# Kernel optimization log

Measured on AMD Instinct MI355X. Metric: run time of the kernel, lower is better.

The kernel has to match this reference:

```python
import jax, jax.numpy as jnp
import numpy as np

N = 10000        # nodes
E = 320000       # edges (before self-loops)
IN = 128         # in_channels
HID = 128        # hidden_channels per head
HEADS = 4
OUT = 512        # out_channels (final layer, 1 head, no concat)
SLOPE = 0.2      # PyG GATConv negative_slope default


def setup_inputs() -> dict:
    key = jax.random.key(0)
    ks = jax.random.split(key, 16)
    s = 0.05
    inp = {
        "x": jax.random.normal(ks[0], (N, IN), dtype=jnp.float32),
        "edge_index": jax.random.randint(ks[1], (2, E), 0, N, dtype=jnp.int32),
        # layer 1: IN -> HEADS*HID, concat
        "W1": jax.random.normal(ks[2], (IN, HEADS * HID), dtype=jnp.float32) * s,
        "a_src1": jax.random.normal(ks[3], (1, HEADS, HID), dtype=jnp.float32) * s,
        "a_dst1": jax.random.normal(ks[4], (1, HEADS, HID), dtype=jnp.float32) * s,
        "b1": jnp.zeros((HEADS * HID,), dtype=jnp.float32),
        # layer 2: HEADS*HID -> HEADS*HID, concat
        "W2": jax.random.normal(ks[5], (HEADS * HID, HEADS * HID), dtype=jnp.float32) * s,
        "a_src2": jax.random.normal(ks[6], (1, HEADS, HID), dtype=jnp.float32) * s,
        "a_dst2": jax.random.normal(ks[7], (1, HEADS, HID), dtype=jnp.float32) * s,
        "b2": jnp.zeros((HEADS * HID,), dtype=jnp.float32),
        # layer 3: HEADS*HID -> OUT, heads=1, mean (no concat)
        "W3": jax.random.normal(ks[8], (HEADS * HID, OUT), dtype=jnp.float32) * s,
        "a_src3": jax.random.normal(ks[9], (1, 1, OUT), dtype=jnp.float32) * s,
        "a_dst3": jax.random.normal(ks[10], (1, 1, OUT), dtype=jnp.float32) * s,
        "b3": jnp.zeros((OUT,), dtype=jnp.float32),
    }
    return inp


def gat_layer(x, src, dst, W, a_src, a_dst, bias, heads, ch, concat):
    n = x.shape[0]
    h = (x @ W).reshape(n, heads, ch)                 # [N,H,C]
    al_s = jnp.sum(h * a_src, axis=-1)                # [N,H]
    al_d = jnp.sum(h * a_dst, axis=-1)                # [N,H]
    logits = jax.nn.leaky_relu(al_s[src] + al_d[dst], SLOPE)  # [E,H]
    # segment softmax over incoming edges of each destination node
    logits = logits - jax.ops.segment_max(logits, dst, num_segments=n)[dst]
    e = jnp.exp(logits)
    denom = jax.ops.segment_sum(e, dst, num_segments=n)[dst]
    alpha = e / denom                                  # [E,H]
    out = jax.ops.segment_sum(h[src] * alpha[:, :, None], dst, num_segments=n)  # [N,H,C]
    out = out.reshape(n, heads * ch) if concat else out.mean(axis=1)
    return out + bias


def reference(x, edge_index, W1, a_src1, a_dst1, b1, W2, a_src2, a_dst2, b2,
              W3, a_src3, a_dst3, b3):
    n = x.shape[0]
    loop = jnp.arange(n, dtype=edge_index.dtype)       # PyG add_self_loops=True
    src = jnp.concatenate([edge_index[0], loop])
    dst = jnp.concatenate([edge_index[1], loop])
    h = jax.nn.relu(gat_layer(x, src, dst, W1, a_src1, a_dst1, b1, HEADS, HID, True))
    h = jax.nn.relu(gat_layer(h, src, dst, W2, a_src2, a_dst2, b2, HEADS, HID, True))
    return gat_layer(h, src, dst, W3, a_src3, a_dst3, b3, 1, OUT, False)
```

## Files before the change

### kernel.cpp

```cpp
#include <hip/hip_runtime.h>

#define NSLOPE 0.2f
#define CAP 128

typedef __bf16 bf16x8 __attribute__((ext_vector_type(8)));
typedef __bf16 bf16x4 __attribute__((ext_vector_type(4)));
typedef __bf16 bf16x2 __attribute__((ext_vector_type(2)));
typedef float  f32x4  __attribute__((ext_vector_type(4)));

typedef uint32_t __attribute__((address_space(1))) gbl_u32;
typedef uint32_t __attribute__((address_space(3))) lds_u32;

__global__ void fill_kernel(const int* __restrict__ ei, int E,
                            int* cnt, int* __restrict__ col){
  int i = blockIdx.x*blockDim.x + threadIdx.x;
  if (i < E){
    int s = ei[i], d = ei[E + i];
    int slot = atomicAdd(&cnt[d], 1);
    if (slot < CAP) col[(d << 7) + slot] = s;
  }
}

__device__ __forceinline__ void wsplit_body(
    const float* __restrict__ W, __bf16* __restrict__ Bt, int K, int Nc,
    int kb, int nb, float (*hi_s)[33], float (*lo_s)[33]){
  int tx = threadIdx.x & 31, ty = threadIdx.x >> 5;
  int k0 = kb * 32, n0 = nb * 32;
#pragma unroll
  for (int i = 0; i < 4; i++){
    int r = ty + i*8;
    float v = W[(size_t)(k0 + r)*Nc + n0 + tx];
    float h = (float)(__bf16)v;
    hi_s[r][tx] = h;
    lo_s[r][tx] = v - h;
  }
  __syncthreads();
  int K2 = 2*K;
#pragma unroll
  for (int i = 0; i < 4; i++){
    int n = ty + i*8;
    Bt[(size_t)(n0 + n)*K2 + k0 + tx]     = (__bf16)hi_s[tx][n];
    Bt[(size_t)(n0 + n)*K2 + K + k0 + tx] = (__bf16)lo_s[tx][n];
  }
}

__global__ __launch_bounds__(256) void prep_kernel(
    const float* __restrict__ x, __bf16* __restrict__ X2,
    const float* __restrict__ W1, __bf16* __restrict__ B1t,
    const float* __restrict__ W2, __bf16* __restrict__ B2t,
    const float* __restrict__ W3, __bf16* __restrict__ B3t,
    int* __restrict__ cnt, int* __restrict__ col,
    float* __restrict__ albase, int N){
  __shared__ float hi_s[32][33], lo_s[32][33];
  int b = blockIdx.x, t = threadIdx.x;
  int gid = b*256 + t;
  if (gid < N){
    cnt[gid] = 1;
    col[gid << 7] = gid;
  }
  if (gid*4 < N*18) *(float4*)(albase + gid*4) = make_float4(0.f,0.f,0.f,0.f);

  const int nb_split = (N*32 + 255) / 256;
  if (b < nb_split){
    int i = gid * 4;
    if (i < N*128){
      int n = i >> 7, c = i & 127;
      float4 v = *(const float4*)(x + i);
      float f[4] = {v.x, v.y, v.z, v.w};
      bf16x4 h, l;
#pragma unroll
      for (int u = 0; u < 4; u++){
        __bf16 hh = (__bf16)f[u];
        h[u] = hh;
        l[u] = (__bf16)(f[u] - (float)hh);
      }
      *(bf16x4*)(X2 + (size_t)n*256 + c)       = h;
      *(bf16x4*)(X2 + (size_t)n*256 + 128 + c) = l;
    }
  } else if (b < nb_split + 64){
    int bb = b - nb_split;
    wsplit_body(W1, B1t, 128, 512, bb & 3, bb >> 2, hi_s, lo_s);
  } else if (b < nb_split + 64 + 256){
    int bb = b - nb_split - 64;
    wsplit_body(W2, B2t, 512, 512, bb & 15, bb >> 4, hi_s, lo_s);
  } else {
    int bb = b - nb_split - 320;
    wsplit_body(W3, B3t, 512, 512, bb & 15, bb >> 4, hi_s, lo_s);
  }
}

template<int H>
__global__ __launch_bounds__(256) void gemm_mfma(
    const __bf16* __restrict__ A2, const __bf16* __restrict__ B2t,
    __bf16* __restrict__ Hb, const float* __restrict__ asrc,
    const float* __restrict__ adst, float* __restrict__ al_s,
    float* __restrict__ al_d, int M, int K2){
  __shared__ uint4 As[1024];
  __shared__ uint4 Bs[1024];
  int t = threadIdx.x, w = t >> 6, lane = t & 63;
  int mm = lane & 15, q = lane >> 4;

  int bid = blockIdx.x;
  int rowblk = (bid & 7) + ((bid >> 5) << 3);
  int cb = (bid >> 3) & 3;
  if (rowblk * 128 >= M) return;
  int bm = rowblk * 128;
  int bn = cb * 128;

  const __bf16* gA[4];
  const __bf16* gB[4];
#pragma unroll
  for (int jj = 0; jj < 4; jj++){
    int fb = w*4 + jj;
    int i = fb >> 1, s = fb & 1;
    int rowA = bm + i*16 + mm; rowA = (rowA < M) ? rowA : (M - 1);
    gA[jj] = A2 + (size_t)rowA*K2 + s*32 + q*8;
    int rowB = bn + i*16 + mm;
    gB[jj] = B2t + (size_t)rowB*K2 + s*32 + q*8;
  }

  f32x4 acc[4][4];
#pragma unroll
  for (int i = 0; i < 4; i++)
#pragma unroll
    for (int j = 0; j < 4; j++)
#pragma unroll
      for (int r = 0; r < 4; r++) acc[i][j][r] = 0.f;

  const int niter = K2 >> 6;
  for (int it = 0; it < niter; it++){
    __syncthreads();
#pragma unroll
    for (int jj = 0; jj < 4; jj++){
      int fb = w*4 + jj;
      __builtin_amdgcn_global_load_lds(
          (const gbl_u32*)gA[jj], (lds_u32*)(As + fb*64), 16, 0, 0);
      __builtin_amdgcn_global_load_lds(
          (const gbl_u32*)gB[jj], (lds_u32*)(Bs + fb*64), 16, 0, 0);
      gA[jj] += 64;
      gB[jj] += 64;
    }
    __syncthreads();
#pragma unroll
    for (int s = 0; s < 2; s++){
      bf16x8 af[4], bfr[4];
#pragma unroll
      for (int i2 = 0; i2 < 4; i2++){
        int fbA = ((((w & 1)*4) + i2) << 1) | s;
        af[i2]  = *(bf16x8*)&As[fbA*64 + lane];
        int fbB = ((((w >> 1)*4) + i2) << 1) | s;
        bfr[i2] = *(bf16x8*)&Bs[fbB*64 + lane];
      }
#pragma unroll
      for (int i2 = 0; i2 < 4; i2++)
#pragma unroll
        for (int j2 = 0; j2 < 4; j2++)
          acc[i2][j2] = __builtin_amdgcn_mfma_f32_16x16x32_bf16(
              af[i2], bfr[j2], acc[i2][j2], 0, 0, 0);
    }
  }

  float as_v[4], ad_v[4];
#pragma unroll
  for (int j2 = 0; j2 < 4; j2++){
    int colc = bn + ((w >> 1)*4 + j2)*16 + mm;
    as_v[j2] = asrc[colc];
    ad_v[j2] = adst[colc];
  }
  const int h = (H == 4) ? (bn >> 7) : 0;
#pragma unroll
  for (int i2 = 0; i2 < 4; i2++){
    int rbase = bm + ((w & 1)*4 + i2)*16 + q*4;
#pragma unroll
    for (int j2 = 0; j2 < 4; j2++){
      int colc = bn + ((w >> 1)*4 + j2)*16 + mm;
#pragma unroll
      for (int r = 0; r < 4; r++){
        int row = rbase + r;
        if (row < M) Hb[(size_t)row*512 + colc] = (__bf16)acc[i2][j2][r];
      }
    }
#pragma unroll
    for (int r = 0; r < 4; r++){
      float ps = acc[i2][0][r]*as_v[0] + acc[i2][1][r]*as_v[1]
               + acc[i2][2][r]*as_v[2] + acc[i2][3][r]*as_v[3];
      float pd = acc[i2][0][r]*ad_v[0] + acc[i2][1][r]*ad_v[1]
               + acc[i2][2][r]*ad_v[2] + acc[i2][3][r]*ad_v[3];
#pragma unroll
      for (int off = 1; off < 16; off <<= 1){
        ps += __shfl_xor(ps, off);
        pd += __shfl_xor(pd, off);
      }
      int row = rbase + r;
      if (mm == 0 && row < M){
        atomicAdd(&al_s[(size_t)row*H + h], ps);
        atomicAdd(&al_d[(size_t)row*H + h], pd);
      }
    }
  }
}

template<int H, int MODE>
__global__ __launch_bounds__(64) void aggregate_slice(
    const __bf16* __restrict__ Hb, const float* __restrict__ al_s,
    const float* __restrict__ al_d, const int* __restrict__ cnt,
    const int* __restrict__ col, const float* __restrict__ bias,
    float* __restrict__ outF, __bf16* __restrict__ fhi,
    __bf16* __restrict__ flo, int fstride, int nidx, int N){
  int g = blockIdx.x;
  int x = g & 7, idx = g >> 3;
  int s = x >> 1, half = x & 1;
  int d = half * nidx + idx;
  if (d >= N) return;
  int lane = threadIdx.x;
  int start = d << 7;
  int end = start + cnt[d];
  const int hh = (H == 1) ? 0 : s;
  const float ald = al_d[(size_t)d*H + hh];
  const bf16x2* __restrict__ Hb2 = (const bf16x2*)Hb;
  const size_t coff = s*64 + lane;

  float mx = -1e30f;
  for (int e = start + lane; e < end; e += 64){
    int sc = col[e];
    float v = al_s[(size_t)sc*H + hh] + ald;
    v = (v > 0.f) ? v : NSLOPE * v;
    mx = fmaxf(mx, v);
  }
#pragma unroll
  for (int off = 32; off > 0; off >>= 1)
    mx = fmaxf(mx, __shfl_xor(mx, off));

  __shared__ int   src_s[64];
  __shared__ float a_s[64];

  float ax0=0.f, ay0=0.f, ax1=0.f, ay1=0.f;
  float ax2=0.f, ay2=0.f, ax3=0.f, ay3=0.f;
  float lsum = 0.f;

  for (int c0 = start; c0 < end; c0 += 64){
    int cnt2 = min(64, end - c0);
    if (lane < cnt2){
      int e = c0 + lane;
      int sc = col[e];
      float v = al_s[(size_t)sc*H + hh] + ald;
      v = (v > 0.f) ? v : NSLOPE * v;
      float ev = __expf(v - mx);
      src_s[lane] = sc;
      a_s[lane]   = ev;
      lsum += ev;
    }
    __syncthreads();
    int i = 0;
    for (; i + 4 <= cnt2; i += 4){
      int s0 = src_s[i],   s1 = src_s[i+1];
      int s2 = src_s[i+2], s3 = src_s[i+3];
      float e0 = a_s[i],   e1 = a_s[i+1];
      float e2 = a_s[i+2], e3 = a_s[i+3];
      bf16x2 v0 = Hb2[(size_t)s0*256 + coff];
      bf16x2 v1 = Hb2[(size_t)s1*256 + coff];
      bf16x2 v2 = Hb2[(size_t)s2*256 + coff];
      bf16x2 v3 = Hb2[(size_t)s3*256 + coff];
      ax0 += e0*(float)v0[0]; ay0 += e0*(float)v0[1];
      ax1 += e1*(float)v1[0]; ay1 += e1*(float)v1[1];
      ax2 += e2*(float)v2[0]; ay2 += e2*(float)v2[1];
      ax3 += e3*(float)v3[0]; ay3 += e3*(float)v3[1];
    }
    for (; i < cnt2; i++){
      int s0 = src_s[i];
      float e0 = a_s[i];
      bf16x2 v0 = Hb2[(size_t)s0*256 + coff];
      ax0 += e0*(float)v0[0]; ay0 += e0*(float)v0[1];
    }
    __syncthreads();
  }

#pragma unroll
  for (int off = 32; off > 0; off >>= 1)
    lsum += __shfl_xor(lsum, off);

  float accx = (ax0 + ax1) + (ax2 + ax3);
  float accy = (ay0 + ay1) + (ay2 + ay3);
  float invd = 1.f / lsum;
  int c = s*128 + lane*2;
  float2 bv = *(const float2*)(bias + c);
  float r0 = accx * invd + bv.x;
  float r1 = accy * invd + bv.y;
  if (MODE == 1){
    r0 = fmaxf(r0, 0.f); r1 = fmaxf(r1, 0.f);
    __bf16 h0 = (__bf16)r0, h1 = (__bf16)r1;
    bf16x2 hv; hv[0] = h0; hv[1] = h1;
    bf16x2 lv; lv[0] = (__bf16)(r0 - (float)h0); lv[1] = (__bf16)(r1 - (float)h1);
    *(bf16x2*)(fhi + (size_t)d*fstride + c) = hv;
    *(bf16x2*)(flo + (size_t)d*fstride + c) = lv;
  } else {
    *(float2*)(outF + (size_t)d*512 + c) = make_float2(r0, r1);
  }
}

extern "C" void kernel_launch(void* const* d_in, const int* in_sizes, int n_in,
                              void* d_out, int out_size, void* d_ws, size_t ws_size,
                              hipStream_t stream){
  const float* x   = (const float*)d_in[0];
  const int*   ei  = (const int*)  d_in[1];
  const float* W1  = (const float*)d_in[2];
  const float* as1 = (const float*)d_in[3];
  const float* ad1 = (const float*)d_in[4];
  const float* b1  = (const float*)d_in[5];
  const float* W2  = (const float*)d_in[6];
  const float* as2 = (const float*)d_in[7];
  const float* ad2 = (const float*)d_in[8];
  const float* b2  = (const float*)d_in[9];
  const float* W3  = (const float*)d_in[10];
  const float* as3 = (const float*)d_in[11];
  const float* ad3 = (const float*)d_in[12];
  const float* b3  = (const float*)d_in[13];
  float* out = (float*)d_out;

  const int N = in_sizes[0] / 128;
  const int E = in_sizes[1] / 2;
  const int nidx = (N + 1) / 2;

  __bf16* feat2  = (__bf16*)d_ws;
  __bf16* X2     = feat2 + (size_t)N*1024;
  float*  albase = (float*)(X2 + (size_t)N*256);
  float*  als1   = albase;
  float*  ald1   = als1 + (size_t)N*4;
  float*  als2   = ald1 + (size_t)N*4;
  float*  ald2   = als2 + (size_t)N*4;
  float*  als3   = ald2 + (size_t)N*4;
  float*  ald3   = als3 + (size_t)N;
  int*    cnt    = (int*)(ald3 + (size_t)N);
  int*    col    = cnt + N;
  uintptr_t p  = (uintptr_t)(col + (size_t)N*CAP);
  p = (p + 15) & ~(uintptr_t)15;
  __bf16* B1t = (__bf16*)p;
  __bf16* B2t = B1t + 512*256;
  __bf16* B3t = B2t + 512*1024;
  __bf16* Hb  = B3t + 512*1024;

  const int nb_split = (N*32 + 255)/256;
  const int pgrid = nb_split + 64 + 256 + 256;

  prep_kernel<<<pgrid, 256, 0, stream>>>(x, X2, W1, B1t, W2, B2t, W3, B3t,
                                         cnt, col, albase, N);
  fill_kernel<<<(E+255)/256, 256, 0, stream>>>(ei, E, cnt, col);

  const int nrb = (N + 127)/128;
  const int ggrid = (((nrb + 7) >> 3) << 3) * 4;
  const int agrid = nidx * 8;

  gemm_mfma<4><<<ggrid, 256, 0, stream>>>(X2, B1t, Hb, as1, ad1, als1, ald1, N, 256);
  aggregate_slice<4,1><<<agrid, 64, 0, stream>>>(Hb, als1, ald1, cnt, col, b1,
      (float*)nullptr, feat2, feat2 + 512, 1024, nidx, N);

  gemm_mfma<4><<<ggrid, 256, 0, stream>>>(feat2, B2t, Hb, as2, ad2, als2, ald2, N, 1024);
  aggregate_slice<4,1><<<agrid, 64, 0, stream>>>(Hb, als2, ald2, cnt, col, b2,
      (float*)nullptr, feat2, feat2 + 512, 1024, nidx, N);

  gemm_mfma<1><<<ggrid, 256, 0, stream>>>(feat2, B3t, Hb, as3, ad3, als3, ald3, N, 1024);
  aggregate_slice<1,0><<<agrid, 64, 0, stream>>>(Hb, als3, ald3, cnt, col, b3,
      out, (__bf16*)nullptr, (__bf16*)nullptr, 0, nidx, N);
}
```

Measured before the change: 326.8 us.

## Double-buffer LDS tiles in MFMA GEMM to overlap loads with compute

Doubles the shared-memory A/B tile buffers and restructures the K loop so the next tile is fetched with global_load_lds while MFMAs run on the current tile. Each iteration now uses a single vmcnt wait plus barrier instead of two syncthreads. This is meant to hide global-memory latency in the GEMM stages. In exchange it doubles LDS use, which may reduce occupancy. There is also a possible race, because LDS reads of the current buffer may not be waited on before the next iteration's loads overwrite that buffer.

```diff
diff --git a/kernel.cpp b/kernel.cpp
--- a/kernel.cpp
+++ b/kernel.cpp
@@ -95,8 +95,8 @@
     __bf16* __restrict__ Hb, const float* __restrict__ asrc,
     const float* __restrict__ adst, float* __restrict__ al_s,
     float* __restrict__ al_d, int M, int K2){
-  __shared__ uint4 As[1024];
-  __shared__ uint4 Bs[1024];
+  __shared__ uint4 As[2048];
+  __shared__ uint4 Bs[2048];
   int t = threadIdx.x, w = t >> 6, lane = t & 63;
   int mm = lane & 15, q = lane >> 4;
 
@@ -127,38 +127,53 @@
 #pragma unroll
       for (int r = 0; r < 4; r++) acc[i][j][r] = 0.f;
 
+#define STAGE(buf)                                                          \
+  _Pragma("unroll")                                                         \
+  for (int jj = 0; jj < 4; jj++){                                           \
+    int fb = w*4 + jj;                                                      \
+    __builtin_amdgcn_global_load_lds(                                       \
+        (const gbl_u32*)gA[jj], (lds_u32*)(As + (buf)*1024 + fb*64), 16, 0, 0); \
+    __builtin_amdgcn_global_load_lds(                                       \
+        (const gbl_u32*)gB[jj], (lds_u32*)(Bs + (buf)*1024 + fb*64), 16, 0, 0); \
+    gA[jj] += 64;                                                           \
+    gB[jj] += 64;                                                           \
+  }
+
+#define COMPUTE(buf)                                                        \
+  _Pragma("unroll")                                                         \
+  for (int s = 0; s < 2; s++){                                              \
+    bf16x8 af[4], bfr[4];                                                   \
+    _Pragma("unroll")                                                       \
+    for (int i2 = 0; i2 < 4; i2++){                                         \
+      int fbA = ((((w & 1)*4) + i2) << 1) | s;                              \
+      af[i2]  = *(bf16x8*)&As[(buf)*1024 + fbA*64 + lane];                  \
+      int fbB = ((((w >> 1)*4) + i2) << 1) | s;                             \
+      bfr[i2] = *(bf16x8*)&Bs[(buf)*1024 + fbB*64 + lane];                  \
+    }                                                                       \
+    _Pragma("unroll")                                                       \
+    for (int i2 = 0; i2 < 4; i2++)                                          \
+      _Pragma("unroll")                                                     \
+      for (int j2 = 0; j2 < 4; j2++)                                        \
+        acc[i2][j2] = __builtin_amdgcn_mfma_f32_16x16x32_bf16(              \
+            af[i2], bfr[j2], acc[i2][j2], 0, 0, 0);                         \
+  }
+
   const int niter = K2 >> 6;
-  for (int it = 0; it < niter; it++){
-    __syncthreads();
-#pragma unroll
-    for (int jj = 0; jj < 4; jj++){
-      int fb = w*4 + jj;
-      __builtin_amdgcn_global_load_lds(
-          (const gbl_u32*)gA[jj], (lds_u32*)(As + fb*64), 16, 0, 0);
-      __builtin_amdgcn_global_load_lds(
-          (const gbl_u32*)gB[jj], (lds_u32*)(Bs + fb*64), 16, 0, 0);
-      gA[jj] += 64;
-      gB[jj] += 64;
-    }
-    __syncthreads();
-#pragma unroll
-    for (int s = 0; s < 2; s++){
-      bf16x8 af[4], bfr[4];
-#pragma unroll
-      for (int i2 = 0; i2 < 4; i2++){
-        int fbA = ((((w & 1)*4) + i2) << 1) | s;
-        af[i2]  = *(bf16x8*)&As[fbA*64 + lane];
-        int fbB = ((((w >> 1)*4) + i2) << 1) | s;
-        bfr[i2] = *(bf16x8*)&Bs[fbB*64 + lane];
-      }
-#pragma unroll
-      for (int i2 = 0; i2 < 4; i2++)
-#pragma unroll
-        for (int j2 = 0; j2 < 4; j2++)
-          acc[i2][j2] = __builtin_amdgcn_mfma_f32_16x16x32_bf16(
-              af[i2], bfr[j2], acc[i2][j2], 0, 0, 0);
-    }
-  }
+  STAGE(0);
+  asm volatile("s_waitcnt vmcnt(0)" ::: "memory");
+  __builtin_amdgcn_s_barrier();
+  int cur = 0;
+  for (int it = 0; it < niter - 1; it++){
+    STAGE(cur ^ 1);
+    COMPUTE(cur);
+    asm volatile("s_waitcnt vmcnt(0)" ::: "memory");
+    __builtin_amdgcn_s_barrier();
+    cur ^= 1;
+  }
+  COMPUTE(cur);
+
+#undef STAGE
+#undef COMPUTE
 
   float as_v[4], ad_v[4];
 #pragma unroll
```

New measurement: 344.2 us. +5.3%, slower.
